# Optimization experiments

Hardware: AMD Instinct MI355X
Metric: run time of the kernel (lower is better)

## Reference

```python
import jax, jax.numpy as jnp
import numpy as np

N_NODES = 50000
N_EDGES = 800000
F_IN = 128
UNIQUE_USER = 64
HIDDEN = 64
HEADS = 4


def _glorot(key, shape):
    fan_in, fan_out = shape[0], shape[-1]
    lim = (6.0 / (fan_in + fan_out)) ** 0.5
    return jax.random.uniform(key, shape, jnp.float32, -lim, lim)


def setup_inputs() -> dict:
    key = jax.random.key(0)
    ks = jax.random.split(key, 16)
    x = jax.random.normal(ks[0], (N_NODES, F_IN), jnp.float32)
    edge_index = jax.random.randint(ks[1], (2, N_EDGES), 0, N_NODES, jnp.int64)
    return {
        "x": x,
        "edge_index": edge_index,
        # lazy Linear layers (PyG Linear: y = x @ W + b)
        "lin1_w": _glorot(ks[2], (F_IN, UNIQUE_USER)),
        "lin1_b": jnp.zeros((UNIQUE_USER,), jnp.float32),
        "lin2_w": _glorot(ks[3], (F_IN, HIDDEN)),
        "lin2_b": jnp.zeros((HIDDEN,), jnp.float32),
        "lin3_w": _glorot(ks[4], (HIDDEN, HIDDEN)),
        "lin3_b": jnp.zeros((HIDDEN,), jnp.float32),
        # FeaStConv 1: in=UNIQUE_USER, out=HIDDEN, heads=HEADS
        "conv1_w": _glorot(ks[5], (UNIQUE_USER, HEADS * HIDDEN)),
        "conv1_u": _glorot(ks[6], (UNIQUE_USER, HEADS)),
        "conv1_c": jnp.zeros((HEADS,), jnp.float32),
        "conv1_bias": jnp.zeros((HIDDEN,), jnp.float32),
        # FeaStConv 2: in=HIDDEN, out=HIDDEN, heads=HEADS
        "conv2_w": _glorot(ks[7], (HIDDEN, HEADS * HIDDEN)),
        "conv2_u": _glorot(ks[8], (HIDDEN, HEADS)),
        "conv2_c": jnp.zeros((HEADS,), jnp.float32),
        "conv2_bias": jnp.zeros((HIDDEN,), jnp.float32),
    }


def feast_conv(x, edge_index, w, u, c, bias):
    # PyG FeaStConv, add_self_loops=False, aggr='mean'
    src, dst = edge_index[0], edge_index[1]  # message flows src(j) -> dst(i)
    x_j = x[src]                              # [E, Fin] gather
    x_i = x[dst]                              # [E, Fin] gather
    heads = u.shape[1]
    out_ch = w.shape[1] // heads
    # attention over heads: q = softmax((x_j - x_i) @ u + c)
    q = jax.nn.softmax((x_j - x_i) @ u + c, axis=-1)          # [E, H]
    w3 = w.reshape(w.shape[0], heads, out_ch)                  # [Fin, H, D]
    # message_e = sum_h q[e,h] * (x_j[e] @ W_h)
    msg = jnp.einsum('ef,fhd,eh->ed', x_j, w3, q)              # [E, D]
    agg = jax.ops.segment_sum(msg, dst, num_segments=N_NODES)  # [N, D]
    cnt = jax.ops.segment_sum(jnp.ones((msg.shape[0],), msg.dtype), dst,
                              num_segments=N_NODES)
    out = agg / jnp.clip(cnt, 1.0)[:, None]
    return out + bias


def reference(x, edge_index, lin1_w, lin1_b, lin2_w, lin2_b, lin3_w, lin3_b,
              conv1_w, conv1_u, conv1_c, conv1_bias,
              conv2_w, conv2_u, conv2_c, conv2_bias):
    h = feast_conv(x @ lin1_w + lin1_b, edge_index,
                   conv1_w, conv1_u, conv1_c, conv1_bias) + (x @ lin2_w + lin2_b)
    h = jax.nn.relu(h)
    h = feast_conv(h, edge_index,
                   conv2_w, conv2_u, conv2_c, conv2_bias) + (h @ lin3_w + lin3_b)
    return jax.nn.relu(h)
```

## Files before the change

kernel.cpp:

```cpp
#include <hip/hip_runtime.h>

#define NN 50000
#define NE 800000
#define NBUCK ((NN + 255) / 256)
#define EPB 4096
#define BCAP 8192
#define QCAP 512

typedef unsigned int uint32;
typedef unsigned short ushort16;
typedef __attribute__((ext_vector_type(8))) short bf16x8;
typedef __attribute__((ext_vector_type(4))) float f32x4;

__device__ __forceinline__ ushort16 f2bf(float f) {
    uint32 u = __float_as_uint(f);
    u += 0x7fff + ((u >> 16) & 1);
    return (ushort16)(u >> 16);
}
__device__ __forceinline__ float bf_lo(uint32 u) {
    return __uint_as_float(u << 16);
}
__device__ __forceinline__ float bf_hi(uint32 u) {
    return __uint_as_float(u & 0xffff0000u);
}
__device__ __forceinline__ bf16x8 pack8(const float4 a, const float4 b) {
    union { bf16x8 v; ushort16 u[8]; } r;
    r.u[0] = f2bf(a.x); r.u[1] = f2bf(a.y); r.u[2] = f2bf(a.z); r.u[3] = f2bf(a.w);
    r.u[4] = f2bf(b.x); r.u[5] = f2bf(b.y); r.u[6] = f2bf(b.z); r.u[7] = f2bf(b.w);
    return r.v;
}
__device__ __forceinline__ float4 softq(const float4 ts, const float4 td,
                                        const float4 tc, const float invdeg) {
    const float l0 = ts.x - td.x + tc.x;
    const float l1 = ts.y - td.y + tc.y;
    const float l2 = ts.z - td.z + tc.z;
    const float l3 = ts.w - td.w + tc.w;
    const float mx = fmaxf(fmaxf(l0, l1), fmaxf(l2, l3));
    const float e0 = __expf(l0 - mx);
    const float e1 = __expf(l1 - mx);
    const float e2 = __expf(l2 - mx);
    const float e3 = __expf(l3 - mx);
    const float sden = invdeg / (e0 + e1 + e2 + e3);
    return make_float4(e0 * sden, e1 * sden, e2 * sden, e3 * sden);
}

__device__ __forceinline__ float multireduce16(const float* tl, int m) {
    float t8[8];
#pragma unroll
    for (int i = 0; i < 8; ++i) {
        const float a0 = tl[2 * i], b0 = tl[2 * i + 1];
        const float oa = __shfl_xor(a0, 1, 64), ob = __shfl_xor(b0, 1, 64);
        t8[i] = ((m & 1) == 0) ? (a0 + oa) : (b0 + ob);
    }
    float t4[4];
#pragma unroll
    for (int i = 0; i < 4; ++i) {
        const float a0 = t8[2 * i], b0 = t8[2 * i + 1];
        const float oa = __shfl_xor(a0, 2, 64), ob = __shfl_xor(b0, 2, 64);
        t4[i] = ((m & 2) == 0) ? (a0 + oa) : (b0 + ob);
    }
    float t2[2];
#pragma unroll
    for (int i = 0; i < 2; ++i) {
        const float a0 = t4[2 * i], b0 = t4[2 * i + 1];
        const float oa = __shfl_xor(a0, 4, 64), ob = __shfl_xor(b0, 4, 64);
        t2[i] = ((m & 4) == 0) ? (a0 + oa) : (b0 + ob);
    }
    const float a0 = t2[0], b0 = t2[1];
    const float oa = __shfl_xor(a0, 8, 64), ob = __shfl_xor(b0, 8, 64);
    return ((m & 8) == 0) ? (a0 + oa) : (b0 + ob);
}

__device__ __forceinline__ ushort16 packp_val(const float* __restrict__ w, int i) {
    const int j  = i & 7;
    const int ln = (i >> 3) & 63;
    const int s  = (i >> 9) & 7;
    const int cc = i >> 12;
    const int k  = s * 32 + ((ln >> 4) * 8) + j;
    const int n  = cc * 16 + (ln & 15);
    return f2bf(w[(k >> 2) * 256 + (k & 3) * 64 + n]);
}

__global__ __launch_bounds__(256) void k_packall(
    const float* __restrict__ w1, const float* __restrict__ w2,
    const float* __restrict__ wc1, const float* __restrict__ wc2,
    const float* __restrict__ wl3,
    ushort16* __restrict__ pw12, ushort16* __restrict__ pwc1,
    ushort16* __restrict__ pwc2, ushort16* __restrict__ pwl3,
    int* __restrict__ bcnt)
{
    const int gid = blockIdx.x * 256 + threadIdx.x;
    if (gid < 16384) {
        const int i = gid;
        const int j  = i & 7;
        const int ln = (i >> 3) & 63;
        const int s  = (i >> 9) & 3;
        const int cc = i >> 11;
        const int k  = s * 32 + ((ln >> 4) * 8) + j;
        const int n  = cc * 16 + (ln & 15);
        pw12[i] = f2bf((n < 64) ? w1[k * 64 + n] : w2[k * 64 + (n - 64)]);
    } else if (gid < 32768) {
        pwc1[gid - 16384] = packp_val(wc1, gid - 16384);
    } else if (gid < 49152) {
        pwc2[gid - 32768] = packp_val(wc2, gid - 32768);
    } else if (gid < 53248) {
        const int i = gid - 49152;
        const int j  = i & 7;
        const int ln = (i >> 3) & 63;
        const int s  = (i >> 9) & 1;
        const int cc = i >> 10;
        const int k  = s * 32 + ((ln >> 4) * 8) + j;
        const int n  = cc * 16 + (ln & 15);
        pwl3[i] = f2bf(wl3[k * 64 + n]);
    } else if (gid < 53504) {
        bcnt[gid - 53248] = 0;
    }
}

__global__ __launch_bounds__(256) void k_lin12(
    const float* __restrict__ x, const ushort16* __restrict__ pw,
    const float* __restrict__ b1, const float* __restrict__ b2,
    const float* __restrict__ u,
    ushort16* __restrict__ ab, float* __restrict__ skip,
    float* __restrict__ tOut)
{
    const int tid = threadIdx.x;
    const int lane = tid & 63;
    const int g = tid >> 6;
    const int m = lane & 15;
    const int quad = lane >> 4;
    const int rowBase = blockIdx.x * 64 + g * 16;

    const int arow = min(rowBase + m, NN - 1);
    const float* xr = x + (size_t)arow * 128 + quad * 8;

    f32x4 acc[8];
#pragma unroll
    for (int c = 0; c < 8; ++c)
#pragma unroll
        for (int r = 0; r < 4; ++r) acc[c][r] = 0.f;

#pragma unroll
    for (int s = 0; s < 4; ++s) {
        const float4 xa = *(const float4*)(xr + s * 32);
        const float4 xb = *(const float4*)(xr + s * 32 + 4);
        const bf16x8 af = pack8(xa, xb);
#pragma unroll
        for (int c = 0; c < 8; ++c) {
            const bf16x8 bf = *(const bf16x8*)&pw[((c * 4 + s) * 64 + lane) * 8];
            acc[c] = __builtin_amdgcn_mfma_f32_16x16x32_bf16(af, bf, acc[c], 0, 0, 0);
        }
    }

    float tl[16];
#pragma unroll
    for (int i = 0; i < 16; ++i) tl[i] = 0.f;

#pragma unroll
    for (int c = 0; c < 8; ++c) {
        const int colg = c * 16 + m;
        const float bv = (colg < 64) ? b1[colg] : b2[colg - 64];
#pragma unroll
        for (int reg = 0; reg < 4; ++reg) {
            const float v = acc[c][reg] + bv;
            const int gr = rowBase + quad * 4 + reg;
            if (gr < NN) {
                if (c < 4) ab[gr * 64 + colg] = f2bf(v);
                else       skip[gr * 64 + (colg - 64)] = v;
            }
            if (c < 4) {
                const float4 uv = ((const float4*)u)[colg];
                tl[reg * 4 + 0] += v * uv.x;
                tl[reg * 4 + 1] += v * uv.y;
                tl[reg * 4 + 2] += v * uv.z;
                tl[reg * 4 + 3] += v * uv.w;
            }
        }
    }

    const float tv = multireduce16(tl, m);
    const int gidx = rowBase * 4 + (quad << 4) + m;
    if (gidx < NN * 4) tOut[gidx] = tv;
}

__global__ __launch_bounds__(256) void k_bin(const int* __restrict__ ei,
                                             int* __restrict__ bcnt,
                                             uint32* __restrict__ pairs)
{
    __shared__ int hist[NBUCK];
    __shared__ int gbase[NBUCK];
    const int t = threadIdx.x;
    const int base = blockIdx.x * EPB;

    for (int b = t; b < NBUCK; b += 256) hist[b] = 0;
    __syncthreads();

    uint32 pk[16];
    int bk[16], rk[16];
#pragma unroll
    for (int k = 0; k < 16; ++k) {
        const int e = base + k * 256 + t;
        if (e < NE) {
            const int s = ei[e];
            const int d = ei[NE + e];
            bk[k] = d >> 8;
            pk[k] = (uint32)s | ((uint32)(d & 255) << 16);
            rk[k] = atomicAdd(&hist[bk[k]], 1);
        }
    }
    __syncthreads();

    for (int b = t; b < NBUCK; b += 256)
        gbase[b] = hist[b] ? atomicAdd(&bcnt[b], hist[b]) : 0;
    __syncthreads();

#pragma unroll
    for (int k = 0; k < 16; ++k) {
        const int e = base + k * 256 + t;
        if (e < NE) pairs[(size_t)bk[k] * BCAP + gbase[bk[k]] + rk[k]] = pk[k];
    }
}

__global__ __launch_bounds__(256) void k_binscat(const uint32* __restrict__ pairs,
                                                 const int* __restrict__ bcnt,
                                                 int* __restrict__ row_ptr,
                                                 int* __restrict__ ssrc)
{
    __shared__ int sb[256];
    __shared__ int hist[256];
    __shared__ int s[256];
    __shared__ int lptr[256];
    __shared__ int lcur[256];
    const int b = blockIdx.x;
    const int t = threadIdx.x;
    const int total = bcnt[b];
    const uint32* pb = pairs + (size_t)b * BCAP;

    sb[t] = (t < NBUCK) ? bcnt[t] : 0;
    __syncthreads();
    for (int off = 1; off < 256; off <<= 1) {
        const int v = (t >= off) ? sb[t - off] : 0;
        __syncthreads();
        sb[t] += v;
        __syncthreads();
    }
    const int base = sb[b] - total;
    if (b == 0 && t == 0) row_ptr[NN] = NE;

    hist[t] = 0;
    __syncthreads();
    for (int e = t; e < total; e += 256) atomicAdd(&hist[pb[e] >> 16], 1);
    __syncthreads();

    const int v = hist[t];
    s[t] = v;
    __syncthreads();
    for (int off = 1; off < 256; off <<= 1) {
        const int u = (t >= off) ? s[t - off] : 0;
        __syncthreads();
        s[t] += u;
        __syncthreads();
    }
    const int excl = base + s[t] - v;
    lptr[t] = excl;
    lcur[t] = 0;
    const int n = (b << 8) + t;
    if (n < NN) row_ptr[n] = excl;
    __syncthreads();

    for (int e = t; e < total; e += 256) {
        const uint32 p = pb[e];
        const int d = p >> 16;
        const int r = atomicAdd(&lcur[d], 1);
        ssrc[lptr[d] + r] = (int)(p & 0xffffu);
    }
}

__global__ __launch_bounds__(256) void k_aggpost(
    const int* __restrict__ row_ptr, const int* __restrict__ ssrc,
    const float* __restrict__ t, const uint32* __restrict__ abu,
    const float* __restrict__ c,
    const ushort16* __restrict__ pw, const float* __restrict__ bias,
    float* skip,
    float* __restrict__ out, ushort16* __restrict__ outb,
    const float* __restrict__ uproj, float* __restrict__ tOut,
    const ushort16* __restrict__ pwl3, const float* __restrict__ b3)
{
    __shared__ float4 ql[QCAP];
    __shared__ char zl[16 * 512];
    __shared__ char hl[16 * 128];
    __shared__ float t_lds[4][64];
    __shared__ float4 tnode[16];
    __shared__ float invdegs[16];

    const int tid = threadIdx.x;
    const int lane = tid & 63;
    const int w = tid >> 6;
    const int qtr = lane >> 4;
    const int u4 = lane & 15;
    const int nodeBase = blockIdx.x * 16;

    const float4 tc = *(const float4*)c;
    const uint2* ab8 = (const uint2*)abu;

    int rr = 0;
    if (lane < 7) {
        const int off = (lane < 5) ? (w * 4 + lane) : ((lane == 5) ? 0 : 16);
        rr = row_ptr[nodeBase + off];
    }
    const int rp0 = __shfl(rr, 0, 64);
    const int rp1 = __shfl(rr, 1, 64);
    const int rp2 = __shfl(rr, 2, 64);
    const int rp3 = __shfl(rr, 3, 64);
    const int rp4 = __shfl(rr, 4, 64);
    const int r0b = __shfl(rr, 5, 64);
    const int r1b = __shfl(rr, 6, 64);

    if (lane < 4) {
        tnode[w * 4 + lane] = ((const float4*)t)[nodeBase + w * 4 + lane];
        const int a = (lane == 0) ? rp0 : (lane == 1) ? rp1 : (lane == 2) ? rp2 : rp3;
        const int b = (lane == 0) ? rp1 : (lane == 1) ? rp2 : (lane == 2) ? rp3 : rp4;
        invdegs[w * 4 + lane] = (b > a) ? 1.f / (float)(b - a) : 0.f;
    }

    const bool fit = (r1b - r0b) <= QCAP;

    if (fit) {
        for (int i = rp0 + lane; i < rp4; i += 64) {
            const int se = ssrc[i];
            const int dl = (i >= rp1) + (i >= rp2) + (i >= rp3);
            const float4 ts = ((const float4*)t)[se];
            const float4 q = softq(ts, tnode[w * 4 + dl], tc, invdegs[w * 4 + dl]);
            ql[i - r0b] = make_float4(q.y, q.z, q.w, __int_as_float(se));
        }
    }

#define ACCQ(QA, AV)                                                   \
    {                                                                  \
        const float q1 = (QA).x, q2 = (QA).y, q3 = (QA).z;             \
        const float q0 = invdeg - q1 - q2 - q3;                        \
        const float v0 = bf_lo((AV).x), v1 = bf_hi((AV).x);            \
        const float v2 = bf_lo((AV).y), v3 = bf_hi((AV).y);            \
        z[0] += q0 * v0;  z[1] += q0 * v1;  z[2] += q0 * v2;  z[3] += q0 * v3;  \
        z[4] += q1 * v0;  z[5] += q1 * v1;  z[6] += q1 * v2;  z[7] += q1 * v3;  \
        z[8] += q2 * v0;  z[9] += q2 * v1;  z[10] += q2 * v2; z[11] += q2 * v3; \
        z[12] += q3 * v0; z[13] += q3 * v1; z[14] += q3 * v2; z[15] += q3 * v3; \
    }
#define ACCQ4(Q4, AV)                                                  \
    {                                                                  \
        const float v0 = bf_lo((AV).x), v1 = bf_hi((AV).x);            \
        const float v2 = bf_lo((AV).y), v3 = bf_hi((AV).y);            \
        z[0] += (Q4).x * v0;  z[1] += (Q4).x * v1;  z[2] += (Q4).x * v2;  z[3] += (Q4).x * v3;  \
        z[4] += (Q4).y * v0;  z[5] += (Q4).y * v1;  z[6] += (Q4).y * v2;  z[7] += (Q4).y * v3;  \
        z[8] += (Q4).z * v0;  z[9] += (Q4).z * v1;  z[10] += (Q4).z * v2; z[11] += (Q4).z * v3; \
        z[12] += (Q4).w * v0; z[13] += (Q4).w * v1; z[14] += (Q4).w * v2; z[15] += (Q4).w * v3; \
    }

#pragma unroll
    for (int nn = 0; nn < 4; ++nn) {
        const int nloc = w * 4 + nn;
        const int r0 = (nn == 0) ? rp0 : (nn == 1) ? rp1 : (nn == 2) ? rp2 : rp3;
        const int r1 = (nn == 0) ? rp1 : (nn == 1) ? rp2 : (nn == 2) ? rp3 : rp4;
        const float invdeg = (r1 > r0) ? 1.f / (float)(r1 - r0) : 0.f;

        float z[16];
#pragma unroll
        for (int i = 0; i < 16; ++i) z[i] = 0.f;

        if (fit) {
            const float4* qb = ql - r0b;
            int idx = r0;
            for (; idx + 7 < r1; idx += 8) {
                const float4 qa0 = qb[idx + qtr];
                const float4 qa1 = qb[idx + 4 + qtr];
                const uint2 av0 = ab8[__float_as_int(qa0.w) * 16 + u4];
                const uint2 av1 = ab8[__float_as_int(qa1.w) * 16 + u4];
                ACCQ(qa0, av0) ACCQ(qa1, av1)
            }
            if (idx + qtr < r1) {
                const float4 qa = qb[idx + qtr];
                const uint2 av = ab8[__float_as_int(qa.w) * 16 + u4];
                ACCQ(qa, av)
            }
            if (idx + 4 + qtr < r1) {
                const float4 qa = qb[idx + 4 + qtr];
                const uint2 av = ab8[__float_as_int(qa.w) * 16 + u4];
                ACCQ(qa, av)
            }
        } else {
            const float4 td = tnode[nloc];
            for (int idx = r0; idx < r1; idx += 4) {
                const int e = idx + qtr;
                if (e < r1) {
                    const int se = ssrc[e];
                    const uint2 av = ab8[se * 16 + u4];
                    const float4 q4 = softq(((const float4*)t)[se], td, tc, invdeg);
                    ACCQ4(q4, av)
                }
            }
        }
#undef ACCQ
#undef ACCQ4

#pragma unroll
        for (int i = 0; i < 16; ++i) {
            z[i] += __shfl_xor(z[i], 16, 64);
            z[i] += __shfl_xor(z[i], 32, 64);
        }

        if (qtr == 0) {
            uint4 pk;
            pk.x = (uint32)f2bf(z[0])  | ((uint32)f2bf(z[4])  << 16);
            pk.y = (uint32)f2bf(z[8])  | ((uint32)f2bf(z[12]) << 16);
            pk.z = (uint32)f2bf(z[1])  | ((uint32)f2bf(z[5])  << 16);
            pk.w = (uint32)f2bf(z[9])  | ((uint32)f2bf(z[13]) << 16);
            *(uint4*)(zl + nloc * 512 + (((2 * u4) * 16) ^ ((nloc & 7) << 4))) = pk;
        } else if (qtr == 1) {
            uint4 pk;
            pk.x = (uint32)f2bf(z[2])  | ((uint32)f2bf(z[6])  << 16);
            pk.y = (uint32)f2bf(z[10]) | ((uint32)f2bf(z[14]) << 16);
            pk.z = (uint32)f2bf(z[3])  | ((uint32)f2bf(z[7])  << 16);
            pk.w = (uint32)f2bf(z[11]) | ((uint32)f2bf(z[15]) << 16);
            *(uint4*)(zl + nloc * 512 + (((2 * u4 + 1) * 16) ^ ((nloc & 7) << 4))) = pk;
        }
    }
    __syncthreads();

    const int m = lane & 15;
    const int quad = lane >> 4;

    f32x4 acc;
#pragma unroll
    for (int r = 0; r < 4; ++r) acc[r] = 0.f;

#pragma unroll
    for (int s = 0; s < 8; ++s) {
        const bf16x8 af = *(const bf16x8*)(zl + m * 512 +
                            ((s * 64 + quad * 16) ^ ((m & 7) << 4)));
        const bf16x8 bf = *(const bf16x8*)&pw[((w * 8 + s) * 64 + lane) * 8];
        acc = __builtin_amdgcn_mfma_f32_16x16x32_bf16(af, bf, acc, 0, 0, 0);
    }

    const int colg = w * 16 + m;
    const float bv = bias[colg];

    float tl[16];
#pragma unroll
    for (int i = 0; i < 16; ++i) tl[i] = 0.f;

#pragma unroll
    for (int reg = 0; reg < 4; ++reg) {
        const int gr = nodeBase + quad * 4 + reg;
        const float v = fmaxf(acc[reg] + bv + skip[gr * 64 + colg], 0.f);
        if (out)  out[gr * 64 + colg]  = v;
        if (outb) outb[gr * 64 + colg] = f2bf(v);
        if (pwl3) {
            const int row = quad * 4 + reg;
            *(ushort16*)(hl + ((row * 128 + colg * 2) ^ ((row & 7) << 4))) = f2bf(v);
        }
        if (tOut) {
            const float4 uv = ((const float4*)uproj)[colg];
            tl[reg * 4 + 0] += v * uv.x;
            tl[reg * 4 + 1] += v * uv.y;
            tl[reg * 4 + 2] += v * uv.z;
            tl[reg * 4 + 3] += v * uv.w;
        }
    }

    if (tOut) {
        const float tv = multireduce16(tl, m);
        t_lds[w][lane] = tv;
    }
    __syncthreads();

    if (tOut && w == 0) {
        const float tvf = t_lds[0][lane] + t_lds[1][lane] +
                          t_lds[2][lane] + t_lds[3][lane];
        tOut[nodeBase * 4 + lane] = tvf;
    }

    if (pwl3) {
        f32x4 acc3;
#pragma unroll
        for (int r = 0; r < 4; ++r) acc3[r] = 0.f;
#pragma unroll
        for (int s = 0; s < 2; ++s) {
            const bf16x8 af = *(const bf16x8*)(hl +
                                ((m * 128 + quad * 16 + s * 64) ^ ((m & 7) << 4)));
            const bf16x8 bf = *(const bf16x8*)&pwl3[((w * 2 + s) * 64 + lane) * 8];
            acc3 = __builtin_amdgcn_mfma_f32_16x16x32_bf16(af, bf, acc3, 0, 0, 0);
        }
        const float b3v = b3[colg];
#pragma unroll
        for (int reg = 0; reg < 4; ++reg) {
            const int gr = nodeBase + quad * 4 + reg;
            skip[gr * 64 + colg] = acc3[reg] + b3v;
        }
    }
}

extern "C" void kernel_launch(void* const* d_in, const int* in_sizes, int n_in,
                              void* d_out, int out_size, void* d_ws, size_t ws_size,
                              hipStream_t stream) {
    const float* x       = (const float*)d_in[0];
    const int*   ei      = (const int*)d_in[1];
    const float* lin1_w  = (const float*)d_in[2];
    const float* lin1_b  = (const float*)d_in[3];
    const float* lin2_w  = (const float*)d_in[4];
    const float* lin2_b  = (const float*)d_in[5];
    const float* lin3_w  = (const float*)d_in[6];
    const float* lin3_b  = (const float*)d_in[7];
    const float* conv1_w = (const float*)d_in[8];
    const float* conv1_u = (const float*)d_in[9];
    const float* conv1_c = (const float*)d_in[10];
    const float* conv1_bias = (const float*)d_in[11];
    const float* conv2_w = (const float*)d_in[12];
    const float* conv2_u = (const float*)d_in[13];
    const float* conv2_c = (const float*)d_in[14];
    const float* conv2_bias = (const float*)d_in[15];
    float* out = (float*)d_out;

    char* p = (char*)d_ws;
    float* skip   = (float*)p;           p += (size_t)NN * 64 * 4;
    float* tt     = (float*)p;           p += (size_t)NN * 4 * 4;
    float* tt2    = (float*)p;           p += (size_t)NN * 4 * 4;
    ushort16* ab  = (ushort16*)p;        p += (size_t)NN * 64 * 2;
    ushort16* hb  = (ushort16*)p;        p += (size_t)NN * 64 * 2;
    ushort16* pw12 = (ushort16*)p;       p += 16384 * 2;
    ushort16* pwc1 = (ushort16*)p;       p += 16384 * 2;
    ushort16* pwc2 = (ushort16*)p;       p += 16384 * 2;
    ushort16* pwl3 = (ushort16*)p;       p += 4096 * 2;
    int* ssrc     = (int*)p;             p += (size_t)NE * 4;
    int* row_ptr  = (int*)p;             p += (size_t)(NN + 1) * 4;
    int* bcnt     = (int*)p;             p += 256 * 4;
    uint32* pairs = (uint32*)p;          p += (size_t)NBUCK * BCAP * 4;

    k_packall<<<209, 256, 0, stream>>>(lin1_w, lin2_w, conv1_w, conv2_w, lin3_w,
                                       pw12, pwc1, pwc2, pwl3, bcnt);
    k_bin<<<(NE + EPB - 1) / EPB, 256, 0, stream>>>(ei, bcnt, pairs);
    k_binscat<<<NBUCK, 256, 0, stream>>>(pairs, bcnt, row_ptr, ssrc);

    k_lin12<<<(NN + 63) / 64, 256, 0, stream>>>(x, pw12, lin1_b, lin2_b, conv1_u,
                                                ab, skip, tt);
    k_aggpost<<<NN / 16, 256, 0, stream>>>(row_ptr, ssrc, tt,
                                           (const uint32*)ab, conv1_c,
                                           pwc1, conv1_bias, skip,
                                           nullptr, hb, conv2_u, tt2,
                                           pwl3, lin3_b);

    k_aggpost<<<NN / 16, 256, 0, stream>>>(row_ptr, ssrc, tt2,
                                           (const uint32*)hb, conv2_c,
                                           pwc2, conv2_bias, skip,
                                           out, nullptr, nullptr, nullptr,
                                           nullptr, nullptr);
}
```

Measured before the change: 218.6 us.

## Halve nodes per aggregation block and unroll edge gather four-wide

Each k_aggpost block now handles 8 nodes instead of 16, two per wave, which doubles the grid to spread the irregular gather work over more blocks. The upper half of the 16-row MFMA tile is zero-padded in LDS, and output stores are limited to the valid rows. The edge loop now issues four predicated neighbour loads per iteration and drops the remainder tail, to raise memory-level parallelism. In exchange, half of the MFMA and epilogue work is wasted on padding, and per-block fixed overhead such as weight loads is paid twice as often.

```diff
diff --git a/kernel.cpp b/kernel.cpp
--- a/kernel.cpp
+++ b/kernel.cpp
@@ -290,47 +290,48 @@
     __shared__ char zl[16 * 512];
     __shared__ char hl[16 * 128];
     __shared__ float t_lds[4][64];
-    __shared__ float4 tnode[16];
-    __shared__ float invdegs[16];
+    __shared__ float4 tnode[8];
+    __shared__ float invdegs[8];
 
     const int tid = threadIdx.x;
     const int lane = tid & 63;
     const int w = tid >> 6;
     const int qtr = lane >> 4;
     const int u4 = lane & 15;
-    const int nodeBase = blockIdx.x * 16;
+    const int nodeBase = blockIdx.x * 8;
+
+    *(uint4*)(zl + 8 * 512 + tid * 16) = make_uint4(0, 0, 0, 0);
+    if (tid < 64) *(uint4*)(hl + 8 * 128 + tid * 16) = make_uint4(0, 0, 0, 0);
 
     const float4 tc = *(const float4*)c;
     const uint2* ab8 = (const uint2*)abu;
 
     int rr = 0;
-    if (lane < 7) {
-        const int off = (lane < 5) ? (w * 4 + lane) : ((lane == 5) ? 0 : 16);
+    if (lane < 5) {
+        const int off = (lane < 3) ? (w * 2 + lane) : ((lane == 3) ? 0 : 8);
         rr = row_ptr[nodeBase + off];
     }
     const int rp0 = __shfl(rr, 0, 64);
     const int rp1 = __shfl(rr, 1, 64);
     const int rp2 = __shfl(rr, 2, 64);
-    const int rp3 = __shfl(rr, 3, 64);
-    const int rp4 = __shfl(rr, 4, 64);
-    const int r0b = __shfl(rr, 5, 64);
-    const int r1b = __shfl(rr, 6, 64);
-
-    if (lane < 4) {
-        tnode[w * 4 + lane] = ((const float4*)t)[nodeBase + w * 4 + lane];
-        const int a = (lane == 0) ? rp0 : (lane == 1) ? rp1 : (lane == 2) ? rp2 : rp3;
-        const int b = (lane == 0) ? rp1 : (lane == 1) ? rp2 : (lane == 2) ? rp3 : rp4;
-        invdegs[w * 4 + lane] = (b > a) ? 1.f / (float)(b - a) : 0.f;
+    const int r0b = __shfl(rr, 3, 64);
+    const int r1b = __shfl(rr, 4, 64);
+
+    if (lane < 2) {
+        tnode[w * 2 + lane] = ((const float4*)t)[nodeBase + w * 2 + lane];
+        const int a = (lane == 0) ? rp0 : rp1;
+        const int b = (lane == 0) ? rp1 : rp2;
+        invdegs[w * 2 + lane] = (b > a) ? 1.f / (float)(b - a) : 0.f;
     }
 
     const bool fit = (r1b - r0b) <= QCAP;
 
     if (fit) {
-        for (int i = rp0 + lane; i < rp4; i += 64) {
+        for (int i = rp0 + lane; i < rp2; i += 64) {
             const int se = ssrc[i];
-            const int dl = (i >= rp1) + (i >= rp2) + (i >= rp3);
+            const int dl = (i >= rp1);
             const float4 ts = ((const float4*)t)[se];
-            const float4 q = softq(ts, tnode[w * 4 + dl], tc, invdegs[w * 4 + dl]);
+            const float4 q = softq(ts, tnode[w * 2 + dl], tc, invdegs[w * 2 + dl]);
             ql[i - r0b] = make_float4(q.y, q.z, q.w, __int_as_float(se));
         }
     }
@@ -357,10 +358,10 @@
     }
 
 #pragma unroll
-    for (int nn = 0; nn < 4; ++nn) {
-        const int nloc = w * 4 + nn;
-        const int r0 = (nn == 0) ? rp0 : (nn == 1) ? rp1 : (nn == 2) ? rp2 : rp3;
-        const int r1 = (nn == 0) ? rp1 : (nn == 1) ? rp2 : (nn == 2) ? rp3 : rp4;
+    for (int nn = 0; nn < 2; ++nn) {
+        const int nloc = w * 2 + nn;
+        const int r0 = (nn == 0) ? rp0 : rp1;
+        const int r1 = (nn == 0) ? rp1 : rp2;
         const float invdeg = (r1 > r0) ? 1.f / (float)(r1 - r0) : 0.f;
 
         float z[16];
@@ -369,23 +370,25 @@
 
         if (fit) {
             const float4* qb = ql - r0b;
-            int idx = r0;
-            for (; idx + 7 < r1; idx += 8) {
-                const float4 qa0 = qb[idx + qtr];
-                const float4 qa1 = qb[idx + 4 + qtr];
+            for (int idx = r0; idx < r1; idx += 16) {
+                const int e0 = idx + qtr;
+                const int e1 = idx + 4 + qtr;
+                const int e2 = idx + 8 + qtr;
+                const int e3 = idx + 12 + qtr;
+                const bool k0 = e0 < r1, k1 = e1 < r1;
+                const bool k2 = e2 < r1, k3 = e3 < r1;
+                const float4 qa0 = qb[k0 ? e0 : r0];
+                const float4 qa1 = qb[k1 ? e1 : r0];
+                const float4 qa2 = qb[k2 ? e2 : r0];
+                const float4 qa3 = qb[k3 ? e3 : r0];
                 const uint2 av0 = ab8[__float_as_int(qa0.w) * 16 + u4];
                 const uint2 av1 = ab8[__float_as_int(qa1.w) * 16 + u4];
-                ACCQ(qa0, av0) ACCQ(qa1, av1)
-            }
-            if (idx + qtr < r1) {
-                const float4 qa = qb[idx + qtr];
-                const uint2 av = ab8[__float_as_int(qa.w) * 16 + u4];
-                ACCQ(qa, av)
-            }
-            if (idx + 4 + qtr < r1) {
-                const float4 qa = qb[idx + 4 + qtr];
-                const uint2 av = ab8[__float_as_int(qa.w) * 16 + u4];
-                ACCQ(qa, av)
+                const uint2 av2 = ab8[__float_as_int(qa2.w) * 16 + u4];
+                const uint2 av3 = ab8[__float_as_int(qa3.w) * 16 + u4];
+                if (k0) ACCQ(qa0, av0)
+                if (k1) ACCQ(qa1, av1)
+                if (k2) ACCQ(qa2, av2)
+                if (k3) ACCQ(qa3, av3)
             }
         } else {
             const float4 td = tnode[nloc];
@@ -448,22 +451,24 @@
 #pragma unroll
     for (int i = 0; i < 16; ++i) tl[i] = 0.f;
 
-#pragma unroll
-    for (int reg = 0; reg < 4; ++reg) {
-        const int gr = nodeBase + quad * 4 + reg;
-        const float v = fmaxf(acc[reg] + bv + skip[gr * 64 + colg], 0.f);
-        if (out)  out[gr * 64 + colg]  = v;
-        if (outb) outb[gr * 64 + colg] = f2bf(v);
-        if (pwl3) {
-            const int row = quad * 4 + reg;
-            *(ushort16*)(hl + ((row * 128 + colg * 2) ^ ((row & 7) << 4))) = f2bf(v);
-        }
-        if (tOut) {
-            const float4 uv = ((const float4*)uproj)[colg];
-            tl[reg * 4 + 0] += v * uv.x;
-            tl[reg * 4 + 1] += v * uv.y;
-            tl[reg * 4 + 2] += v * uv.z;
-            tl[reg * 4 + 3] += v * uv.w;
+    if (quad < 2) {
+#pragma unroll
+        for (int reg = 0; reg < 4; ++reg) {
+            const int gr = nodeBase + quad * 4 + reg;
+            const float v = fmaxf(acc[reg] + bv + skip[gr * 64 + colg], 0.f);
+            if (out)  out[gr * 64 + colg]  = v;
+            if (outb) outb[gr * 64 + colg] = f2bf(v);
+            if (pwl3) {
+                const int row = quad * 4 + reg;
+                *(ushort16*)(hl + ((row * 128 + colg * 2) ^ ((row & 7) << 4))) = f2bf(v);
+            }
+            if (tOut) {
+                const float4 uv = ((const float4*)uproj)[colg];
+                tl[reg * 4 + 0] += v * uv.x;
+                tl[reg * 4 + 1] += v * uv.y;
+                tl[reg * 4 + 2] += v * uv.z;
+                tl[reg * 4 + 3] += v * uv.w;
+            }
         }
     }
 
@@ -473,7 +478,7 @@
     }
     __syncthreads();
 
-    if (tOut && w == 0) {
+    if (tOut && w == 0 && lane < 32) {
         const float tvf = t_lds[0][lane] + t_lds[1][lane] +
                           t_lds[2][lane] + t_lds[3][lane];
         tOut[nodeBase * 4 + lane] = tvf;
@@ -490,11 +495,13 @@
             const bf16x8 bf = *(const bf16x8*)&pwl3[((w * 2 + s) * 64 + lane) * 8];
             acc3 = __builtin_amdgcn_mfma_f32_16x16x32_bf16(af, bf, acc3, 0, 0, 0);
         }
-        const float b3v = b3[colg];
-#pragma unroll
-        for (int reg = 0; reg < 4; ++reg) {
-            const int gr = nodeBase + quad * 4 + reg;
-            skip[gr * 64 + colg] = acc3[reg] + b3v;
+        if (quad < 2) {
+            const float b3v = b3[colg];
+#pragma unroll
+            for (int reg = 0; reg < 4; ++reg) {
+                const int gr = nodeBase + quad * 4 + reg;
+                skip[gr * 64 + colg] = acc3[reg] + b3v;
+            }
         }
     }
 }
@@ -542,15 +549,15 @@
 
     k_lin12<<<(NN + 63) / 64, 256, 0, stream>>>(x, pw12, lin1_b, lin2_b, conv1_u,
                                                 ab, skip, tt);
-    k_aggpost<<<NN / 16, 256, 0, stream>>>(row_ptr, ssrc, tt,
-                                           (const uint32*)ab, conv1_c,
-                                           pwc1, conv1_bias, skip,
-                                           nullptr, hb, conv2_u, tt2,
-                                           pwl3, lin3_b);
-
-    k_aggpost<<<NN / 16, 256, 0, stream>>>(row_ptr, ssrc, tt2,
-                                           (const uint32*)hb, conv2_c,
-                                           pwc2, conv2_bias, skip,
-                                           out, nullptr, nullptr, nullptr,
-                                           nullptr, nullptr);
-}
+    k_aggpost<<<NN / 8, 256, 0, stream>>>(row_ptr, ssrc, tt,
+                                          (const uint32*)ab, conv1_c,
+                                          pwc1, conv1_bias, skip,
+                                          nullptr, hb, conv2_u, tt2,
+                                          pwl3, lin3_b);
+
+    k_aggpost<<<NN / 8, 256, 0, stream>>>(row_ptr, ssrc, tt2,
+                                          (const uint32*)hb, conv2_c,
+                                          pwc2, conv2_bias, skip,
+                                          out, nullptr, nullptr, nullptr,
+                                          nullptr, nullptr);
+}
```

Measured after the change: 231.8 us. 1.06x slower.
